# Kernel tuning notes

Hardware: AMD Instinct MI355X
Metric: run time of the kernel (lower is better)

## Reference

```python
import jax, jax.numpy as jnp
import numpy as np

N_NODES = 4194304  # 2**22
LEVELS = 10
COARSE = 8192
RANK = 2
NNZ = 8388608


def _interp_linear(u, N):
    """torch F.interpolate(mode='linear', align_corners=False) along axis 1. u: (B,M,R) -> (B,N,R)."""
    M = u.shape[1]
    pos = (jnp.arange(N, dtype=jnp.float32) + 0.5) * (M / N) - 0.5
    pos = jnp.clip(pos, 0.0, M - 1)
    i0 = jnp.floor(pos).astype(jnp.int32)
    i1 = jnp.minimum(i0 + 1, M - 1)
    w = (pos - i0.astype(jnp.float32))[None, :, None]
    return u[:, i0] * (1.0 - w) + u[:, i1] * w


def _apply_hodlr(diag, u_factors, v_factors, x):
    B, N, _ = x.shape
    y = diag * x
    L = u_factors.shape[0]
    for lvl in range(L):
        num_splits = 2 ** (lvl + 1)
        bs = N // num_splits
        if bs == 0:
            continue
        uc, vc = u_factors[lvl], v_factors[lvl]
        u_full = _interp_linear(uc, N) if uc.shape[1] != N else uc
        v_full = _interp_linear(vc, N) if vc.shape[1] != N else vc
        P = num_splits // 2
        valid = P * 2 * bs
        xv = x[:, :valid].reshape(B, P, 2, bs, 1)
        uv = u_full[:, :valid].reshape(B, P, 2, bs, -1)
        vv = v_full[:, :valid].reshape(B, P, 2, bs, -1)
        xL, xR = xv[:, :, 0], xv[:, :, 1]
        uL, uR = uv[:, :, 0], uv[:, :, 1]
        vL, vR = vv[:, :, 0], vv[:, :, 1]
        xRp = jnp.einsum('bpkr,bpko->bpro', vR, xR)  # (B,P,R,1)
        xLp = jnp.einsum('bpkr,bpko->bpro', vL, xL)
        yL = jnp.einsum('bpkr,bpro->bpko', uL, xRp)  # (B,P,bs,1)
        yR = jnp.einsum('bpkr,bpro->bpko', uR, xLp)
        upd = jnp.stack([yL, yR], axis=2).reshape(B, valid, 1)
        if valid < N:
            upd = jnp.pad(upd, ((0, 0), (0, N - valid), (0, 0)))
        y = y + upd
    return y


def setup_inputs() -> dict:
    key = jax.random.key(0)
    ks = jax.random.split(key, 6)
    diag = jax.random.uniform(ks[0], (1, N_NODES, 1), dtype=jnp.float32)
    u_factors = jax.random.normal(ks[1], (LEVELS, 1, COARSE, RANK), dtype=jnp.float32)
    v_factors = jax.random.normal(ks[2], (LEVELS, 1, COARSE, RANK), dtype=jnp.float32)
    A_values = jax.random.normal(ks[3], (NNZ,), dtype=jnp.float32)
    z = jax.random.normal(ks[4], (1, N_NODES, 1), dtype=jnp.float32)
    A_indices = jax.random.randint(ks[5], (2, NNZ), 0, N_NODES, dtype=jnp.int64) if jax.config.jax_enable_x64 else jax.random.randint(ks[5], (2, NNZ), 0, N_NODES, dtype=jnp.int32)
    return {"diag": diag, "u_factors": u_factors, "v_factors": v_factors,
            "A_values": A_values, "z": z, "A_indices": A_indices, "num_nodes": N_NODES}


def reference(diag, u_factors, v_factors, A_values, z, A_indices, num_nodes):
    N = num_nodes
    w = _apply_hodlr(diag, u_factors, v_factors, z)          # (1,N,1)
    w_flat = w.reshape(N)
    rows, cols = A_indices[0], A_indices[1]
    y_flat = jax.ops.segment_sum(A_values * w_flat[cols], rows, num_segments=N)
    y = y_flat.reshape(1, N, 1)
    loss = jnp.mean((y - z) ** 2)
    return loss
```

## Files before the change

kernel.cpp:

```cpp
#include <hip/hip_runtime.h>

#define N_NODES 4194304
#define LEVELS  10
#define COARSE  8192
#define NNZ_E   8388608
#define NCHUNK  16384
#define NB      256
#define BROWS   16384
#define BSH     14
#define HB      2048
#define EPB     4096

typedef int          v4i __attribute__((ext_vector_type(4)));
typedef float        v4f __attribute__((ext_vector_type(4)));
typedef unsigned int v4u __attribute__((ext_vector_type(4)));

static __device__ __forceinline__ unsigned short f2bf(float x) {
    unsigned u = __float_as_uint(x);
    return (unsigned short)((u + 0x7FFFu + ((u >> 16) & 1u)) >> 16);
}
static __device__ __forceinline__ float bf2f(unsigned short h) {
    return __uint_as_float((unsigned)h << 16);
}
static __device__ __forceinline__ unsigned f18(float p) {
    return ((__float_as_uint(p) + 0x2000u) >> 14) & 0x3FFFFu;
}

__global__ __launch_bounds__(256) void kD1(const float* __restrict__ z,
                                           float2* __restrict__ M,
                                           float* __restrict__ S,
                                           float* __restrict__ out,
                                           const int* __restrict__ rows,
                                           unsigned* __restrict__ blockOff) {
    int b = blockIdx.x, t = threadIdx.x;
    if (b < 4096) {
        if (b == 0) {
            for (int i = t; i < 2046 * 2; i += 256) S[i] = 0.f;
            if (t == 0) out[0] = 0.f;
        }
        int lane = t & 63, wave = t >> 6;
        int chunk = b * 4 + wave;
        int base = chunk * 256 + lane * 4;
        float4 zv = *(const float4*)(z + base);
        float a0 = 0.f, a1 = 0.f;
        const float* zp = (const float*)&zv;
#pragma unroll
        for (int j = 0; j < 4; ++j) {
            float p = ((float)(base + j) + 0.5f) * (1.0f / 512.0f) - 0.5f;
            p = fminf(fmaxf(p, 0.0f), (float)(COARSE - 1));
            float f = p - floorf(p);
            a0 += zp[j] * (1.0f - f);
            a1 += zp[j] * f;
        }
#pragma unroll
        for (int off = 32; off >= 1; off >>= 1) {
            a0 += __shfl_xor(a0, off, 64);
            a1 += __shfl_xor(a1, off, 64);
        }
        if (lane == 0) M[chunk] = make_float2(a0, a1);
    } else {
        __shared__ unsigned h[NB];
        int blk = b - 4096;
        h[t] = 0u;
        __syncthreads();
        int base = blk * EPB;
#pragma unroll
        for (int it = 0; it < 4; ++it) {
            int e = base + it * 1024 + t * 4;
            v4i r = __builtin_nontemporal_load((const v4i*)(rows + e));
            atomicAdd(&h[r.x >> BSH], 1u); atomicAdd(&h[r.y >> BSH], 1u);
            atomicAdd(&h[r.z >> BSH], 1u); atomicAdd(&h[r.w >> BSH], 1u);
        }
        __syncthreads();
        blockOff[t * HB + blk] = h[t];
    }
}

__global__ __launch_bounds__(256) void kD2(const float2* __restrict__ M,
                                           const float* __restrict__ V,
                                           float* __restrict__ S,
                                           unsigned* __restrict__ blockOff,
                                           unsigned* __restrict__ total) {
    int b = blockIdx.x, t = threadIdx.x;
    if (b < 80) {
        int lvl = b >> 3, slice = b & 7;
        const float2* Vl = (const float2*)(V + lvl * COARSE * 2);
        float s0 = 0.f, s1 = 0.f;
        int c0 = slice * 2048 + t * 8;
#pragma unroll
        for (int cc = 0; cc < 8; ++cc) {
            int c = c0 + cc;
            float2 m = M[c];
            int k = (c > 0) ? ((c - 1) >> 1) : 0;
            int kp = min(k + 1, COARSE - 1);
            float2 vk = Vl[k], vkp = Vl[kp];
            s0 += vk.x * m.x + vkp.x * m.y;
            s1 += vk.y * m.x + vkp.y * m.y;
        }
        int gw = min(1 << (10 - lvl), 64);
        for (int sh = gw >> 1; sh >= 1; sh >>= 1) {
            s0 += __shfl_xor(s0, sh, 64);
            s1 += __shfl_xor(s1, sh, 64);
        }
        if ((t & (gw - 1)) == 0) {
            int bb = c0 >> (13 - lvl);
            int soff = (2 << lvl) - 2;
            unsafeAtomicAdd(&S[(soff + bb) * 2 + 0], s0);
            unsafeAtomicAdd(&S[(soff + bb) * 2 + 1], s1);
        }
    } else {
        int bb = b - 80;
        __shared__ unsigned wsum[4], wbase[4];
        unsigned* p = blockOff + bb * HB;
        v4u a = *(const v4u*)(p + t * 8);
        v4u c = *(const v4u*)(p + t * 8 + 4);
        unsigned s = a.x + a.y + a.z + a.w + c.x + c.y + c.z + c.w;
        unsigned incl = s;
#pragma unroll
        for (int off = 1; off < 64; off <<= 1) {
            unsigned n = __shfl_up(incl, off, 64);
            if ((t & 63) >= off) incl += n;
        }
        if ((t & 63) == 63) wsum[t >> 6] = incl;
        __syncthreads();
        if (t == 0) {
            unsigned acc = 0;
            for (int i = 0; i < 4; ++i) { wbase[i] = acc; acc += wsum[i]; }
            total[bb] = acc;
        }
        __syncthreads();
        unsigned excl = wbase[t >> 6] + incl - s;
        v4u e0, e1;
        e0.x = excl;       e0.y = e0.x + a.x; e0.z = e0.y + a.y; e0.w = e0.z + a.z;
        e1.x = e0.w + a.w; e1.y = e1.x + c.x; e1.z = e1.y + c.y; e1.w = e1.z + c.z;
        *(v4u*)(p + t * 8) = e0;
        *(v4u*)(p + t * 8 + 4) = e1;
    }
}

__global__ __launch_bounds__(256) void kD3(const float* __restrict__ diag,
                                           const float* __restrict__ z,
                                           const float* __restrict__ S,
                                           const float* __restrict__ U,
                                           unsigned short* __restrict__ wb) {
    int tid = blockIdx.x * 256 + threadIdx.x;
    int base = tid * 4;
    int c = base >> 8;
    int k = (c > 0) ? ((c - 1) >> 1) : 0;
    int kp = min(k + 1, COARSE - 1);
    float g0 = 0.f, g1 = 0.f;
#pragma unroll
    for (int lvl = 0; lvl < LEVELS; ++lvl) {
        int sib = (c >> (13 - lvl)) ^ 1;
        int soff = (2 << lvl) - 2;
        float2 s2 = ((const float2*)S)[soff + sib];
        const float2* Ul = (const float2*)(U + lvl * COARSE * 2);
        float2 uk = Ul[k], ukp = Ul[kp];
        g0 += uk.x * s2.x + uk.y * s2.y;
        g1 += ukp.x * s2.x + ukp.y * s2.y;
    }
    float4 d4 = *(const float4*)(diag + base);
    float4 z4 = *(const float4*)(z + base);
    const float* dp = (const float*)&d4;
    const float* zp = (const float*)&z4;
    ushort4 h4;
    unsigned short* hp = (unsigned short*)&h4;
#pragma unroll
    for (int j = 0; j < 4; ++j) {
        float p = ((float)(base + j) + 0.5f) * (1.0f / 512.0f) - 0.5f;
        p = fminf(fmaxf(p, 0.0f), (float)(COARSE - 1));
        float f = p - floorf(p);
        hp[j] = f2bf(dp[j] * zp[j] + (g0 + f * (g1 - g0)));
    }
    *(ushort4*)(wb + base) = h4;
}

__global__ __launch_bounds__(256) void kD4(const int* __restrict__ rows,
                                           const int* __restrict__ cols,
                                           const float* __restrict__ vals,
                                           const unsigned short* __restrict__ wb,
                                           const unsigned* __restrict__ blockOff,
                                           const unsigned* __restrict__ total,
                                           unsigned* __restrict__ packed) {
    __shared__ unsigned cur[NB];
    __shared__ unsigned gb[NB];
    __shared__ unsigned wsum[4], wbase[4];
    __shared__ unsigned sortedP[EPB];
    __shared__ unsigned char sortedB[EPB];
    int blk = blockIdx.x, t = threadIdx.x;

    cur[t] = 0u;
    unsigned tv = total[t];
    unsigned incl = tv;
#pragma unroll
    for (int off = 1; off < 64; off <<= 1) {
        unsigned n = __shfl_up(incl, off, 64);
        if ((t & 63) >= off) incl += n;
    }
    if ((t & 63) == 63) wsum[t >> 6] = incl;
    __syncthreads();
    if (t == 0) {
        unsigned a = 0;
        for (int i = 0; i < 4; ++i) { wbase[i] = a; a += wsum[i]; }
    }
    __syncthreads();
    unsigned bucketBase = wbase[t >> 6] + incl - tv;

    int base = blk * EPB;
    v4i r[4], c[4];
    v4f v[4];
#pragma unroll
    for (int j = 0; j < 4; ++j) {
        int e = base + j * 1024 + t * 4;
        r[j] = __builtin_nontemporal_load((const v4i*)(rows + e));
        c[j] = __builtin_nontemporal_load((const v4i*)(cols + e));
        v[j] = __builtin_nontemporal_load((const v4f*)(vals + e));
    }
    unsigned short wv[16];
#pragma unroll
    for (int j = 0; j < 4; ++j) {
        const int* cp = (const int*)&c[j];
        wv[j * 4 + 0] = wb[cp[0]];
        wv[j * 4 + 1] = wb[cp[1]];
        wv[j * 4 + 2] = wb[cp[2]];
        wv[j * 4 + 3] = wb[cp[3]];
    }
#pragma unroll
    for (int j = 0; j < 4; ++j) {
        const int* rp = (const int*)&r[j];
        atomicAdd(&cur[rp[0] >> BSH], 1u);
        atomicAdd(&cur[rp[1] >> BSH], 1u);
        atomicAdd(&cur[rp[2] >> BSH], 1u);
        atomicAdd(&cur[rp[3] >> BSH], 1u);
    }
    __syncthreads();
    unsigned lv = cur[t];
    unsigned lincl = lv;
#pragma unroll
    for (int off = 1; off < 64; off <<= 1) {
        unsigned n = __shfl_up(lincl, off, 64);
        if ((t & 63) >= off) lincl += n;
    }
    if ((t & 63) == 63) wsum[t >> 6] = lincl;
    __syncthreads();
    if (t == 0) {
        unsigned a = 0;
        for (int i = 0; i < 4; ++i) { wbase[i] = a; a += wsum[i]; }
    }
    __syncthreads();
    unsigned lexcl = wbase[t >> 6] + lincl - lv;
    gb[t] = bucketBase + blockOff[t * HB + blk] - lexcl;
    __syncthreads();
    cur[t] = lexcl;
    __syncthreads();
#pragma unroll
    for (int j = 0; j < 4; ++j) {
        const int* rp = (const int*)&r[j];
        const float* vp = (const float*)&v[j];
#pragma unroll
        for (int kk = 0; kk < 4; ++kk) {
            int row = rp[kk];
            unsigned bkt = (unsigned)row >> BSH;
            float p = vp[kk] * bf2f(wv[j * 4 + kk]);
            unsigned i = atomicAdd(&cur[bkt], 1u);
            sortedP[i] = ((unsigned)(row & (BROWS - 1)) << 18) | f18(p);
            sortedB[i] = (unsigned char)bkt;
        }
    }
    __syncthreads();
#pragma unroll
    for (int k = 0; k < 16; ++k) {
        int i = k * 256 + t;
        unsigned bkt = sortedB[i];
        __builtin_nontemporal_store(sortedP[i], packed + gb[bkt] + i);
    }
}

__global__ __launch_bounds__(1024) void kD5(const unsigned* __restrict__ packed,
                                            const unsigned* __restrict__ total,
                                            const float* __restrict__ z,
                                            float* __restrict__ out) {
    __shared__ float acc[BROWS];
    __shared__ unsigned sb, sn;
    __shared__ unsigned wsum[4], wbase[4];
    __shared__ float red[16];
    int b = blockIdx.x, t = threadIdx.x;

    unsigned tv = 0, incl = 0;
    if (t < 256) {
        tv = total[t];
        incl = tv;
#pragma unroll
        for (int off = 1; off < 64; off <<= 1) {
            unsigned n = __shfl_up(incl, off, 64);
            if ((t & 63) >= off) incl += n;
        }
        if ((t & 63) == 63) wsum[t >> 6] = incl;
    }
    __syncthreads();
    if (t == 0) {
        unsigned a = 0;
        for (int i = 0; i < 4; ++i) { wbase[i] = a; a += wsum[i]; }
    }
    __syncthreads();
    if (t < 256 && t == b) { sb = wbase[t >> 6] + incl - tv; sn = tv; }
    for (int i = t; i < BROWS / 4; i += 1024) ((float4*)acc)[i] = make_float4(0.f, 0.f, 0.f, 0.f);
    __syncthreads();

    unsigned s0 = sb, n = sn;
    for (unsigned i = t; i < n; i += 1024) {
        unsigned e = __builtin_nontemporal_load(packed + s0 + i);
        atomicAdd(&acc[e >> 18], __uint_as_float((e & 0x3FFFFu) << 14));
    }
    __syncthreads();

    float part = 0.f;
    int gbase = b * BROWS;
    for (int i = t; i < BROWS; i += 1024) {
        float d = acc[i] - z[gbase + i];
        part += d * d;
    }
#pragma unroll
    for (int off = 32; off >= 1; off >>= 1) part += __shfl_xor(part, off, 64);
    if ((t & 63) == 0) red[t >> 6] = part;
    __syncthreads();
    if (t == 0) {
        float s = 0.f;
        for (int i = 0; i < 16; ++i) s += red[i];
        unsafeAtomicAdd(out, s * (1.0f / (float)N_NODES));
    }
}

extern "C" void kernel_launch(void* const* d_in, const int* in_sizes, int n_in,
                              void* d_out, int out_size, void* d_ws, size_t ws_size,
                              hipStream_t stream) {
    const float* diag  = (const float*)d_in[0];
    const float* U     = (const float*)d_in[1];
    const float* V     = (const float*)d_in[2];
    const float* Avals = (const float*)d_in[3];
    const float* z     = (const float*)d_in[4];
    const int*   Aidx  = (const int*)d_in[5];
    const int* rows = Aidx;
    const int* cols = Aidx + NNZ_E;

    char* ws = (char*)d_ws;
    size_t off = 0;
    unsigned short* wb = (unsigned short*)(ws + off); off += (size_t)N_NODES * 2;
    unsigned* packed   = (unsigned*)(ws + off);       off += (size_t)NNZ_E * 4;
    unsigned* blockOff = (unsigned*)(ws + off);       off += (size_t)NB * HB * 4;
    unsigned* total    = (unsigned*)(ws + off);       off += 1024;
    float2* M          = (float2*)(ws + off);         off += (size_t)NCHUNK * 8;
    float* S           = (float*)(ws + off);          off += 16384;

    kD1<<<6144, 256, 0, stream>>>(z, M, S, (float*)d_out, rows, blockOff);
    kD2<<<336, 256, 0, stream>>>(M, V, S, blockOff, total);
    kD3<<<4096, 256, 0, stream>>>(diag, z, S, U, wb);
    kD4<<<HB, 256, 0, stream>>>(rows, cols, Avals, wb, blockOff, total, packed);
    kD5<<<NB, 1024, 0, stream>>>(packed, total, z, (float*)d_out);
}
```

Before: 328.0 us.

## Bin edges by column first so the w gather reads from LDS

Adds a column-bucket pass. Edges are first binned by column block into an 8-byte packed record holding the row, the local column and a bf16 value. Each block can then load its 16K-entry slice of w into shared memory and gather from there instead of doing random global reads. The product is then re-binned by row using atomic global row counters, and the final segment-sum kernel is unchanged. This swaps the random global gather for an extra 64MB write and read of binned edges, plus a second histogram over the columns.

```diff
diff --git a/kernel.cpp b/kernel.cpp
--- a/kernel.cpp
+++ b/kernel.cpp
@@ -6,14 +6,16 @@
 #define NNZ_E   8388608
 #define NCHUNK  16384
 #define NB      256
-#define BROWS   16384
-#define BSH     14
-#define HB      2048
-#define EPB     4096
+#define CB_SZ   16384
+#define RB_SZ   16384
+#define HB      1024
+#define EPB     8192
+#define TILE    8192
 
 typedef int          v4i __attribute__((ext_vector_type(4)));
 typedef float        v4f __attribute__((ext_vector_type(4)));
 typedef unsigned int v4u __attribute__((ext_vector_type(4)));
+typedef unsigned int v2u __attribute__((ext_vector_type(2)));
 
 static __device__ __forceinline__ unsigned short f2bf(float x) {
     unsigned u = __float_as_uint(x);
@@ -26,20 +28,22 @@
     return ((__float_as_uint(p) + 0x2000u) >> 14) & 0x3FFFFu;
 }
 
-__global__ __launch_bounds__(256) void kD1(const float* __restrict__ z,
-                                           float2* __restrict__ M,
-                                           float* __restrict__ S,
-                                           float* __restrict__ out,
-                                           const int* __restrict__ rows,
-                                           unsigned* __restrict__ blockOff) {
+__global__ __launch_bounds__(512) void kA(const float* __restrict__ z,
+                                          float2* __restrict__ M,
+                                          float* __restrict__ S,
+                                          float* __restrict__ out,
+                                          const int* __restrict__ rows,
+                                          const int* __restrict__ cols,
+                                          unsigned* __restrict__ colBO,
+                                          unsigned* __restrict__ rowBC) {
     int b = blockIdx.x, t = threadIdx.x;
-    if (b < 4096) {
+    if (b < 2048) {
         if (b == 0) {
-            for (int i = t; i < 2046 * 2; i += 256) S[i] = 0.f;
+            for (int i = t; i < 2046 * 2; i += 512) S[i] = 0.f;
             if (t == 0) out[0] = 0.f;
         }
         int lane = t & 63, wave = t >> 6;
-        int chunk = b * 4 + wave;
+        int chunk = b * 8 + wave;
         int base = chunk * 256 + lane * 4;
         float4 zv = *(const float4*)(z + base);
         float a0 = 0.f, a1 = 0.f;
@@ -59,28 +63,36 @@
         }
         if (lane == 0) M[chunk] = make_float2(a0, a1);
     } else {
-        __shared__ unsigned h[NB];
-        int blk = b - 4096;
-        h[t] = 0u;
+        __shared__ unsigned hc[NB], hr[NB];
+        int blk = b - 2048;
+        if (t < 256) { hc[t] = 0u; hr[t] = 0u; }
         __syncthreads();
         int base = blk * EPB;
 #pragma unroll
         for (int it = 0; it < 4; ++it) {
-            int e = base + it * 1024 + t * 4;
+            int e = base + it * 2048 + t * 4;
             v4i r = __builtin_nontemporal_load((const v4i*)(rows + e));
-            atomicAdd(&h[r.x >> BSH], 1u); atomicAdd(&h[r.y >> BSH], 1u);
-            atomicAdd(&h[r.z >> BSH], 1u); atomicAdd(&h[r.w >> BSH], 1u);
-        }
-        __syncthreads();
-        blockOff[t * HB + blk] = h[t];
-    }
-}
-
-__global__ __launch_bounds__(256) void kD2(const float2* __restrict__ M,
-                                           const float* __restrict__ V,
-                                           float* __restrict__ S,
-                                           unsigned* __restrict__ blockOff,
-                                           unsigned* __restrict__ total) {
+            v4i c = __builtin_nontemporal_load((const v4i*)(cols + e));
+            atomicAdd(&hr[r.x >> 14], 1u); atomicAdd(&hr[r.y >> 14], 1u);
+            atomicAdd(&hr[r.z >> 14], 1u); atomicAdd(&hr[r.w >> 14], 1u);
+            atomicAdd(&hc[c.x >> 14], 1u); atomicAdd(&hc[c.y >> 14], 1u);
+            atomicAdd(&hc[c.z >> 14], 1u); atomicAdd(&hc[c.w >> 14], 1u);
+        }
+        __syncthreads();
+        if (t < 256) {
+            colBO[t * HB + blk] = hc[t];
+            rowBC[t * HB + blk] = hr[t];
+        }
+    }
+}
+
+__global__ __launch_bounds__(256) void kB(const float2* __restrict__ M,
+                                          const float* __restrict__ V,
+                                          float* __restrict__ S,
+                                          unsigned* __restrict__ colBO,
+                                          unsigned* __restrict__ colTotal,
+                                          const unsigned* __restrict__ rowBC,
+                                          unsigned* __restrict__ rowTotal) {
     int b = blockIdx.x, t = threadIdx.x;
     if (b < 80) {
         int lvl = b >> 3, slice = b & 7;
@@ -108,13 +120,12 @@
             unsafeAtomicAdd(&S[(soff + bb) * 2 + 0], s0);
             unsafeAtomicAdd(&S[(soff + bb) * 2 + 1], s1);
         }
-    } else {
+    } else if (b < 336) {
         int bb = b - 80;
         __shared__ unsigned wsum[4], wbase[4];
-        unsigned* p = blockOff + bb * HB;
-        v4u a = *(const v4u*)(p + t * 8);
-        v4u c = *(const v4u*)(p + t * 8 + 4);
-        unsigned s = a.x + a.y + a.z + a.w + c.x + c.y + c.z + c.w;
+        unsigned* p = colBO + bb * HB;
+        v4u a = ((const v4u*)p)[t];
+        unsigned s = a.x + a.y + a.z + a.w;
         unsigned incl = s;
 #pragma unroll
         for (int off = 1; off < 64; off <<= 1) {
@@ -126,188 +137,312 @@
         if (t == 0) {
             unsigned acc = 0;
             for (int i = 0; i < 4; ++i) { wbase[i] = acc; acc += wsum[i]; }
-            total[bb] = acc;
+            colTotal[bb] = acc;
         }
         __syncthreads();
         unsigned excl = wbase[t >> 6] + incl - s;
-        v4u e0, e1;
-        e0.x = excl;       e0.y = e0.x + a.x; e0.z = e0.y + a.y; e0.w = e0.z + a.z;
-        e1.x = e0.w + a.w; e1.y = e1.x + c.x; e1.z = e1.y + c.y; e1.w = e1.z + c.z;
-        *(v4u*)(p + t * 8) = e0;
-        *(v4u*)(p + t * 8 + 4) = e1;
-    }
-}
-
-__global__ __launch_bounds__(256) void kD3(const float* __restrict__ diag,
-                                           const float* __restrict__ z,
-                                           const float* __restrict__ S,
-                                           const float* __restrict__ U,
-                                           unsigned short* __restrict__ wb) {
-    int tid = blockIdx.x * 256 + threadIdx.x;
-    int base = tid * 4;
-    int c = base >> 8;
-    int k = (c > 0) ? ((c - 1) >> 1) : 0;
-    int kp = min(k + 1, COARSE - 1);
-    float g0 = 0.f, g1 = 0.f;
-#pragma unroll
-    for (int lvl = 0; lvl < LEVELS; ++lvl) {
-        int sib = (c >> (13 - lvl)) ^ 1;
-        int soff = (2 << lvl) - 2;
-        float2 s2 = ((const float2*)S)[soff + sib];
-        const float2* Ul = (const float2*)(U + lvl * COARSE * 2);
-        float2 uk = Ul[k], ukp = Ul[kp];
-        g0 += uk.x * s2.x + uk.y * s2.y;
-        g1 += ukp.x * s2.x + ukp.y * s2.y;
-    }
-    float4 d4 = *(const float4*)(diag + base);
-    float4 z4 = *(const float4*)(z + base);
-    const float* dp = (const float*)&d4;
-    const float* zp = (const float*)&z4;
-    ushort4 h4;
-    unsigned short* hp = (unsigned short*)&h4;
-#pragma unroll
-    for (int j = 0; j < 4; ++j) {
-        float p = ((float)(base + j) + 0.5f) * (1.0f / 512.0f) - 0.5f;
-        p = fminf(fmaxf(p, 0.0f), (float)(COARSE - 1));
-        float f = p - floorf(p);
-        hp[j] = f2bf(dp[j] * zp[j] + (g0 + f * (g1 - g0)));
-    }
-    *(ushort4*)(wb + base) = h4;
-}
-
-__global__ __launch_bounds__(256) void kD4(const int* __restrict__ rows,
-                                           const int* __restrict__ cols,
-                                           const float* __restrict__ vals,
-                                           const unsigned short* __restrict__ wb,
-                                           const unsigned* __restrict__ blockOff,
-                                           const unsigned* __restrict__ total,
-                                           unsigned* __restrict__ packed) {
-    __shared__ unsigned cur[NB];
-    __shared__ unsigned gb[NB];
+        v4u e;
+        e.x = excl; e.y = excl + a.x; e.z = e.y + a.y; e.w = e.z + a.z;
+        ((v4u*)p)[t] = e;
+    } else {
+        int bb = b - 336;
+        __shared__ unsigned red[4];
+        v4u vv = ((const v4u*)(rowBC + bb * HB))[t];
+        unsigned s = vv.x + vv.y + vv.z + vv.w;
+#pragma unroll
+        for (int off = 32; off >= 1; off >>= 1) s += __shfl_xor(s, off, 64);
+        if ((t & 63) == 0) red[t >> 6] = s;
+        __syncthreads();
+        if (t == 0) rowTotal[bb] = red[0] + red[1] + red[2] + red[3];
+    }
+}
+
+__global__ __launch_bounds__(512) void kC(const float* __restrict__ diag,
+                                          const float* __restrict__ z,
+                                          const float* __restrict__ S,
+                                          const float* __restrict__ U,
+                                          unsigned short* __restrict__ wb,
+                                          const int* __restrict__ rows,
+                                          const int* __restrict__ cols,
+                                          const float* __restrict__ vals,
+                                          const unsigned* __restrict__ colBO,
+                                          const unsigned* __restrict__ colTotal,
+                                          v2u* __restrict__ colBinned,
+                                          const unsigned* __restrict__ rowTotal,
+                                          unsigned* __restrict__ rowCtr) {
+    int b = blockIdx.x, t = threadIdx.x;
+    if (b < 2048) {
+        int tid = b * 512 + t;
+        int base = tid * 4;
+        int c = base >> 8;
+        int k = (c > 0) ? ((c - 1) >> 1) : 0;
+        int kp = min(k + 1, COARSE - 1);
+        float g0 = 0.f, g1 = 0.f;
+#pragma unroll
+        for (int lvl = 0; lvl < LEVELS; ++lvl) {
+            int sib = (c >> (13 - lvl)) ^ 1;
+            int soff = (2 << lvl) - 2;
+            float2 s2 = ((const float2*)S)[soff + sib];
+            const float2* Ul = (const float2*)(U + lvl * COARSE * 2);
+            float2 uk = Ul[k], ukp = Ul[kp];
+            g0 += uk.x * s2.x + uk.y * s2.y;
+            g1 += ukp.x * s2.x + ukp.y * s2.y;
+        }
+        float4 d4 = *(const float4*)(diag + base);
+        float4 z4 = *(const float4*)(z + base);
+        const float* dp = (const float*)&d4;
+        const float* zp = (const float*)&z4;
+        ushort4 h4;
+        unsigned short* hp = (unsigned short*)&h4;
+#pragma unroll
+        for (int j = 0; j < 4; ++j) {
+            float p = ((float)(base + j) + 0.5f) * (1.0f / 512.0f) - 0.5f;
+            p = fminf(fmaxf(p, 0.0f), (float)(COARSE - 1));
+            float f = p - floorf(p);
+            hp[j] = f2bf(dp[j] * zp[j] + (g0 + f * (g1 - g0)));
+        }
+        *(ushort4*)(wb + base) = h4;
+    } else if (b < 3072) {
+        __shared__ v2u sortedP[EPB];
+        __shared__ unsigned char sortedB[EPB];
+        __shared__ unsigned cur[NB], gb[NB];
+        __shared__ unsigned wsum[4], wbase[4];
+        int blk = b - 2048;
+        int base = blk * EPB;
+        v4i r[4], c[4];
+        v4f v[4];
+#pragma unroll
+        for (int j = 0; j < 4; ++j) {
+            int e = base + j * 2048 + t * 4;
+            r[j] = __builtin_nontemporal_load((const v4i*)(rows + e));
+            c[j] = __builtin_nontemporal_load((const v4i*)(cols + e));
+            v[j] = __builtin_nontemporal_load((const v4f*)(vals + e));
+        }
+        unsigned tv = (t < 256) ? colTotal[t] : 0u;
+        unsigned incl = tv;
+        if (t < 256) {
+#pragma unroll
+            for (int off = 1; off < 64; off <<= 1) {
+                unsigned n = __shfl_up(incl, off, 64);
+                if ((t & 63) >= off) incl += n;
+            }
+            if ((t & 63) == 63) wsum[t >> 6] = incl;
+            cur[t] = 0u;
+        }
+        __syncthreads();
+        if (t == 0) {
+            unsigned a = 0;
+            for (int i = 0; i < 4; ++i) { wbase[i] = a; a += wsum[i]; }
+        }
+        __syncthreads();
+        unsigned segBase = (t < 256) ? (wbase[t >> 6] + incl - tv) : 0u;
+#pragma unroll
+        for (int j = 0; j < 4; ++j) {
+            atomicAdd(&cur[c[j].x >> 14], 1u);
+            atomicAdd(&cur[c[j].y >> 14], 1u);
+            atomicAdd(&cur[c[j].z >> 14], 1u);
+            atomicAdd(&cur[c[j].w >> 14], 1u);
+        }
+        __syncthreads();
+        unsigned lv = (t < 256) ? cur[t] : 0u;
+        unsigned lincl = lv;
+        if (t < 256) {
+#pragma unroll
+            for (int off = 1; off < 64; off <<= 1) {
+                unsigned n = __shfl_up(lincl, off, 64);
+                if ((t & 63) >= off) lincl += n;
+            }
+            if ((t & 63) == 63) wsum[t >> 6] = lincl;
+        }
+        __syncthreads();
+        if (t == 0) {
+            unsigned a = 0;
+            for (int i = 0; i < 4; ++i) { wbase[i] = a; a += wsum[i]; }
+        }
+        __syncthreads();
+        if (t < 256) {
+            unsigned lexcl = wbase[t >> 6] + lincl - lv;
+            gb[t] = segBase + colBO[t * HB + blk] - lexcl;
+            cur[t] = lexcl;
+        }
+        __syncthreads();
+#pragma unroll
+        for (int j = 0; j < 4; ++j) {
+            const int* rp = (const int*)&r[j];
+            const int* cp = (const int*)&c[j];
+            const float* vp = (const float*)&v[j];
+#pragma unroll
+            for (int kk = 0; kk < 4; ++kk) {
+                int row = rp[kk], col = cp[kk];
+                unsigned cb = (unsigned)col >> 14;
+                unsigned cl = (unsigned)col & 16383u;
+                v2u ent;
+                ent.x = (unsigned)row | ((cl & 0x3FFu) << 22);
+                ent.y = (cl >> 10) | ((unsigned)f2bf(vp[kk]) << 16);
+                unsigned i = atomicAdd(&cur[cb], 1u);
+                sortedP[i] = ent;
+                sortedB[i] = (unsigned char)cb;
+            }
+        }
+        __syncthreads();
+#pragma unroll
+        for (int k = 0; k < 16; ++k) {
+            int i = k * 512 + t;
+            unsigned bkt = sortedB[i];
+            __builtin_nontemporal_store(sortedP[i], colBinned + gb[bkt] + i);
+        }
+    } else {
+        __shared__ unsigned wsum[4], wbase[4];
+        unsigned tv = (t < 256) ? rowTotal[t] : 0u;
+        unsigned incl = tv;
+        if (t < 256) {
+#pragma unroll
+            for (int off = 1; off < 64; off <<= 1) {
+                unsigned n = __shfl_up(incl, off, 64);
+                if ((t & 63) >= off) incl += n;
+            }
+            if ((t & 63) == 63) wsum[t >> 6] = incl;
+        }
+        __syncthreads();
+        if (t == 0) {
+            unsigned a = 0;
+            for (int i = 0; i < 4; ++i) { wbase[i] = a; a += wsum[i]; }
+        }
+        __syncthreads();
+        if (t < 256) rowCtr[t] = wbase[t >> 6] + incl - tv;
+    }
+}
+
+__global__ __launch_bounds__(512) void kD(const unsigned short* __restrict__ wb,
+                                          const v2u* __restrict__ colBinned,
+                                          const unsigned* __restrict__ colTotal,
+                                          unsigned* __restrict__ rowCtr,
+                                          unsigned* __restrict__ packed) {
+    __shared__ unsigned short wSl[CB_SZ];
+    __shared__ unsigned sortedP[TILE];
+    __shared__ unsigned char sortedB[TILE];
+    __shared__ unsigned cur[NB], gb[NB];
     __shared__ unsigned wsum[4], wbase[4];
-    __shared__ unsigned sortedP[EPB];
-    __shared__ unsigned char sortedB[EPB];
-    int blk = blockIdx.x, t = threadIdx.x;
-
-    cur[t] = 0u;
-    unsigned tv = total[t];
+    __shared__ unsigned sS;
+    int b = blockIdx.x, t = threadIdx.x;
+
+    unsigned tv = (t < 256) ? colTotal[t] : 0u;
     unsigned incl = tv;
-#pragma unroll
-    for (int off = 1; off < 64; off <<= 1) {
-        unsigned n = __shfl_up(incl, off, 64);
-        if ((t & 63) >= off) incl += n;
-    }
-    if ((t & 63) == 63) wsum[t >> 6] = incl;
+    if (t < 256) {
+#pragma unroll
+        for (int off = 1; off < 64; off <<= 1) {
+            unsigned n = __shfl_up(incl, off, 64);
+            if ((t & 63) >= off) incl += n;
+        }
+        if ((t & 63) == 63) wsum[t >> 6] = incl;
+    }
     __syncthreads();
     if (t == 0) {
         unsigned a = 0;
         for (int i = 0; i < 4; ++i) { wbase[i] = a; a += wsum[i]; }
     }
     __syncthreads();
-    unsigned bucketBase = wbase[t >> 6] + incl - tv;
-
-    int base = blk * EPB;
-    v4i r[4], c[4];
-    v4f v[4];
-#pragma unroll
-    for (int j = 0; j < 4; ++j) {
-        int e = base + j * 1024 + t * 4;
-        r[j] = __builtin_nontemporal_load((const v4i*)(rows + e));
-        c[j] = __builtin_nontemporal_load((const v4i*)(cols + e));
-        v[j] = __builtin_nontemporal_load((const v4f*)(vals + e));
-    }
-    unsigned short wv[16];
-#pragma unroll
-    for (int j = 0; j < 4; ++j) {
-        const int* cp = (const int*)&c[j];
-        wv[j * 4 + 0] = wb[cp[0]];
-        wv[j * 4 + 1] = wb[cp[1]];
-        wv[j * 4 + 2] = wb[cp[2]];
-        wv[j * 4 + 3] = wb[cp[3]];
-    }
-#pragma unroll
-    for (int j = 0; j < 4; ++j) {
-        const int* rp = (const int*)&r[j];
-        atomicAdd(&cur[rp[0] >> BSH], 1u);
-        atomicAdd(&cur[rp[1] >> BSH], 1u);
-        atomicAdd(&cur[rp[2] >> BSH], 1u);
-        atomicAdd(&cur[rp[3] >> BSH], 1u);
-    }
-    __syncthreads();
-    unsigned lv = cur[t];
-    unsigned lincl = lv;
-#pragma unroll
-    for (int off = 1; off < 64; off <<= 1) {
-        unsigned n = __shfl_up(lincl, off, 64);
-        if ((t & 63) >= off) lincl += n;
-    }
-    if ((t & 63) == 63) wsum[t >> 6] = lincl;
+    if (t < 256 && t == b) sS = wbase[t >> 6] + incl - tv;
+    const v4u* wg = (const v4u*)(wb + (size_t)b * CB_SZ);
+    for (int i = t; i < CB_SZ / 8; i += 512) ((v4u*)wSl)[i] = wg[i];
+    __syncthreads();
+    unsigned s0 = sS, n = colTotal[b];
+
+    for (unsigned t0 = 0; t0 < n; t0 += TILE) {
+        unsigned cnt = min((unsigned)TILE, n - t0);
+        if (t < 256) cur[t] = 0u;
+        __syncthreads();
+        v2u ev[16];
+#pragma unroll
+        for (int k = 0; k < 16; ++k) {
+            unsigned i = (unsigned)(k * 512 + t);
+            if (i < cnt) ev[k] = __builtin_nontemporal_load(colBinned + s0 + t0 + i);
+        }
+#pragma unroll
+        for (int k = 0; k < 16; ++k) {
+            if ((unsigned)(k * 512 + t) < cnt)
+                atomicAdd(&cur[(ev[k].x & 0x3FFFFFu) >> 14], 1u);
+        }
+        __syncthreads();
+        unsigned lv = (t < 256) ? cur[t] : 0u;
+        unsigned lincl = lv;
+        if (t < 256) {
+#pragma unroll
+            for (int off = 1; off < 64; off <<= 1) {
+                unsigned nn = __shfl_up(lincl, off, 64);
+                if ((t & 63) >= off) lincl += nn;
+            }
+            if ((t & 63) == 63) wsum[t >> 6] = lincl;
+        }
+        __syncthreads();
+        if (t == 0) {
+            unsigned a = 0;
+            for (int i = 0; i < 4; ++i) { wbase[i] = a; a += wsum[i]; }
+        }
+        __syncthreads();
+        if (t < 256) {
+            unsigned lexcl = wbase[t >> 6] + lincl - lv;
+            gb[t] = atomicAdd(&rowCtr[t], lv) - lexcl;
+            cur[t] = lexcl;
+        }
+        __syncthreads();
+#pragma unroll
+        for (int k = 0; k < 16; ++k) {
+            if ((unsigned)(k * 512 + t) < cnt) {
+                v2u e = ev[k];
+                unsigned row = e.x & 0x3FFFFFu;
+                unsigned cl = (e.x >> 22) | ((e.y & 0xFu) << 10);
+                float p = bf2f((unsigned short)(e.y >> 16)) * bf2f(wSl[cl]);
+                unsigned rb = row >> 14;
+                unsigned i = atomicAdd(&cur[rb], 1u);
+                sortedP[i] = ((row & 16383u) << 18) | f18(p);
+                sortedB[i] = (unsigned char)rb;
+            }
+        }
+        __syncthreads();
+#pragma unroll
+        for (int k = 0; k < 16; ++k) {
+            unsigned i = (unsigned)(k * 512 + t);
+            if (i < cnt) {
+                unsigned bkt = sortedB[i];
+                __builtin_nontemporal_store(sortedP[i], packed + gb[bkt] + i);
+            }
+        }
+        __syncthreads();
+    }
+}
+
+__global__ __launch_bounds__(1024) void kE(const unsigned* __restrict__ packed,
+                                           const unsigned* __restrict__ rowTotal,
+                                           const float* __restrict__ z,
+                                           float* __restrict__ out) {
+    __shared__ float acc[RB_SZ];
+    __shared__ unsigned sb;
+    __shared__ unsigned wsum[4], wbase[4];
+    __shared__ float red[16];
+    int b = blockIdx.x, t = threadIdx.x;
+
+    unsigned tv = (t < 256) ? rowTotal[t] : 0u;
+    unsigned incl = tv;
+    if (t < 256) {
+#pragma unroll
+        for (int off = 1; off < 64; off <<= 1) {
+            unsigned n = __shfl_up(incl, off, 64);
+            if ((t & 63) >= off) incl += n;
+        }
+        if ((t & 63) == 63) wsum[t >> 6] = incl;
+    }
     __syncthreads();
     if (t == 0) {
         unsigned a = 0;
         for (int i = 0; i < 4; ++i) { wbase[i] = a; a += wsum[i]; }
     }
     __syncthreads();
-    unsigned lexcl = wbase[t >> 6] + lincl - lv;
-    gb[t] = bucketBase + blockOff[t * HB + blk] - lexcl;
-    __syncthreads();
-    cur[t] = lexcl;
-    __syncthreads();
-#pragma unroll
-    for (int j = 0; j < 4; ++j) {
-        const int* rp = (const int*)&r[j];
-        const float* vp = (const float*)&v[j];
-#pragma unroll
-        for (int kk = 0; kk < 4; ++kk) {
-            int row = rp[kk];
-            unsigned bkt = (unsigned)row >> BSH;
-            float p = vp[kk] * bf2f(wv[j * 4 + kk]);
-            unsigned i = atomicAdd(&cur[bkt], 1u);
-            sortedP[i] = ((unsigned)(row & (BROWS - 1)) << 18) | f18(p);
-            sortedB[i] = (unsigned char)bkt;
-        }
-    }
-    __syncthreads();
-#pragma unroll
-    for (int k = 0; k < 16; ++k) {
-        int i = k * 256 + t;
-        unsigned bkt = sortedB[i];
-        __builtin_nontemporal_store(sortedP[i], packed + gb[bkt] + i);
-    }
-}
-
-__global__ __launch_bounds__(1024) void kD5(const unsigned* __restrict__ packed,
-                                            const unsigned* __restrict__ total,
-                                            const float* __restrict__ z,
-                                            float* __restrict__ out) {
-    __shared__ float acc[BROWS];
-    __shared__ unsigned sb, sn;
-    __shared__ unsigned wsum[4], wbase[4];
-    __shared__ float red[16];
-    int b = blockIdx.x, t = threadIdx.x;
-
-    unsigned tv = 0, incl = 0;
-    if (t < 256) {
-        tv = total[t];
-        incl = tv;
-#pragma unroll
-        for (int off = 1; off < 64; off <<= 1) {
-            unsigned n = __shfl_up(incl, off, 64);
-            if ((t & 63) >= off) incl += n;
-        }
-        if ((t & 63) == 63) wsum[t >> 6] = incl;
-    }
-    __syncthreads();
-    if (t == 0) {
-        unsigned a = 0;
-        for (int i = 0; i < 4; ++i) { wbase[i] = a; a += wsum[i]; }
-    }
-    __syncthreads();
-    if (t < 256 && t == b) { sb = wbase[t >> 6] + incl - tv; sn = tv; }
-    for (int i = t; i < BROWS / 4; i += 1024) ((float4*)acc)[i] = make_float4(0.f, 0.f, 0.f, 0.f);
-    __syncthreads();
-
-    unsigned s0 = sb, n = sn;
+    if (t < 256 && t == b) sb = wbase[t >> 6] + incl - tv;
+    for (int i = t; i < RB_SZ / 4; i += 1024) ((float4*)acc)[i] = make_float4(0.f, 0.f, 0.f, 0.f);
+    __syncthreads();
+
+    unsigned s0 = sb, n = rowTotal[b];
     for (unsigned i = t; i < n; i += 1024) {
         unsigned e = __builtin_nontemporal_load(packed + s0 + i);
         atomicAdd(&acc[e >> 18], __uint_as_float((e & 0x3FFFFu) << 14));
@@ -315,8 +450,8 @@
     __syncthreads();
 
     float part = 0.f;
-    int gbase = b * BROWS;
-    for (int i = t; i < BROWS; i += 1024) {
+    int gbase = b * RB_SZ;
+    for (int i = t; i < RB_SZ; i += 1024) {
         float d = acc[i] - z[gbase + i];
         part += d * d;
     }
@@ -345,16 +480,21 @@
 
     char* ws = (char*)d_ws;
     size_t off = 0;
-    unsigned short* wb = (unsigned short*)(ws + off); off += (size_t)N_NODES * 2;
-    unsigned* packed   = (unsigned*)(ws + off);       off += (size_t)NNZ_E * 4;
-    unsigned* blockOff = (unsigned*)(ws + off);       off += (size_t)NB * HB * 4;
-    unsigned* total    = (unsigned*)(ws + off);       off += 1024;
-    float2* M          = (float2*)(ws + off);         off += (size_t)NCHUNK * 8;
-    float* S           = (float*)(ws + off);          off += 16384;
-
-    kD1<<<6144, 256, 0, stream>>>(z, M, S, (float*)d_out, rows, blockOff);
-    kD2<<<336, 256, 0, stream>>>(M, V, S, blockOff, total);
-    kD3<<<4096, 256, 0, stream>>>(diag, z, S, U, wb);
-    kD4<<<HB, 256, 0, stream>>>(rows, cols, Avals, wb, blockOff, total, packed);
-    kD5<<<NB, 1024, 0, stream>>>(packed, total, z, (float*)d_out);
-}
+    unsigned short* wb  = (unsigned short*)(ws + off); off += (size_t)N_NODES * 2;
+    v2u* colBinned      = (v2u*)(ws + off);            off += (size_t)NNZ_E * 8;
+    unsigned* packed    = (unsigned*)(ws + off);       off += (size_t)NNZ_E * 4;
+    unsigned* colBO     = (unsigned*)(ws + off);       off += (size_t)NB * HB * 4;
+    unsigned* rowBC     = (unsigned*)(ws + off);       off += (size_t)NB * HB * 4;
+    unsigned* colTotal  = (unsigned*)(ws + off);       off += 1024;
+    unsigned* rowTotal  = (unsigned*)(ws + off);       off += 1024;
+    unsigned* rowCtr    = (unsigned*)(ws + off);       off += 1024;
+    float2* M           = (float2*)(ws + off);         off += (size_t)NCHUNK * 8;
+    float* S            = (float*)(ws + off);          off += 16384;
+
+    kA<<<3072, 512, 0, stream>>>(z, M, S, (float*)d_out, rows, cols, colBO, rowBC);
+    kB<<<592, 256, 0, stream>>>(M, V, S, colBO, colTotal, rowBC, rowTotal);
+    kC<<<3073, 512, 0, stream>>>(diag, z, S, U, wb, rows, cols, Avals,
+                                 colBO, colTotal, colBinned, rowTotal, rowCtr);
+    kD<<<NB, 512, 0, stream>>>(wb, colBinned, colTotal, rowCtr, packed);
+    kE<<<NB, 1024, 0, stream>>>(packed, rowTotal, z, (float*)d_out);
+}
```

After: 311.8 us. 1.05x faster.
